# Kernel optimization log

Measured on AMD Instinct MI355X. Metric: run time of the kernel, lower is better.

Reference implementation:

```python
import jax, jax.numpy as jnp
import numpy as np

N_HEAD = 16

def _alibi_slopes(num_heads):
    # m_i = (256 ** (1/num_heads)) ** -(i+1)
    x = (2.0 ** 8) ** (1.0 / num_heads)
    return jnp.asarray([1.0 / x ** (i + 1) for i in range(num_heads)], dtype=jnp.float32)

def setup_inputs() -> dict:
    key = jax.random.key(0)
    k1, k2 = jax.random.split(key)
    B, S, D = 2, 2048, 1024
    x = jax.random.normal(k1, (B, S, D), dtype=jnp.float32)
    W_kqv = jax.random.normal(k2, (D, 3 * D), dtype=jnp.float32) * 0.02
    return {"x": x, "W_kqv": W_kqv}

def reference(x, W_kqv):
    B, S, D = x.shape
    H = N_HEAD
    hd = D // H
    scale = jnp.sqrt(jnp.asarray(D, dtype=x.dtype))  # NOTE: sqrt(n_embd), per source
    kqv = x @ W_kqv                                   # [B,S,3D]
    k, q, v = jnp.split(kqv, 3, axis=-1)              # chunk order: key, query, value
    q = q.reshape(B, S, H, hd).transpose(0, 2, 1, 3)  # [B,H,S,hd]
    k = k.reshape(B, S, H, hd).transpose(0, 2, 1, 3)
    v = v.reshape(B, S, H, hd).transpose(0, 2, 1, 3)
    # ALiBi bias: m[h] * (j - i)
    pos = jnp.arange(S)
    rel = (pos[None, :] - pos[:, None]).astype(x.dtype)      # [S,S]
    m = _alibi_slopes(H).astype(x.dtype)                     # [H]
    bias = m[:, None, None] * rel                            # [H,S,S]
    score = jnp.einsum('bhqd,bhkd->bhqk', q, k) / scale + bias[None]
    causal = pos[None, :] <= pos[:, None]                    # [S,S] lower-tri
    score = jnp.where(causal[None, None], score, -jnp.inf)
    attn = jax.nn.softmax(score, axis=-1)                    # [B,H,S,S]
    out = jnp.einsum('bhqk,bhkd->bhqd', attn, v)
    out = out.transpose(0, 2, 1, 3).reshape(B, S, D)
    return (out, attn)
```

## Files before the change

kernel.cpp:

```cpp
#include <hip/hip_runtime.h>
#include <hip/hip_bf16.h>

typedef __attribute__((ext_vector_type(8))) short short8;
typedef __attribute__((ext_vector_type(4))) float f32x4;

static __device__ __forceinline__ unsigned short f2bf(float f) {
    unsigned int x = __float_as_uint(f);
    x += 0x7fffu + ((x >> 16) & 1u);
    return (unsigned short)(x >> 16);
}

static __device__ __forceinline__ void gld_lds16(const unsigned short* g, unsigned short* l) {
    __builtin_amdgcn_global_load_lds((const __attribute__((address_space(1))) void*)g,
                                     (__attribute__((address_space(3))) void*)l, 16, 0, 0);
}

__global__ __launch_bounds__(256) void cvt_x_kernel(const float* __restrict__ in,
                                                    unsigned short* __restrict__ outb,
                                                    int n4) {
    int i = blockIdx.x * 256 + threadIdx.x;
    if (i < n4) {
        f32x4 v = *(const f32x4*)(in + (size_t)i * 4);
        ushort4 o;
        o.x = f2bf(v[0]); o.y = f2bf(v[1]); o.z = f2bf(v[2]); o.w = f2bf(v[3]);
        *(ushort4*)(outb + (size_t)i * 4) = o;
    }
}

__global__ __launch_bounds__(256) void cvt_wt_kernel(const float* __restrict__ W,
                                                     unsigned short* __restrict__ WT) {
    __shared__ float t[64][65];
    const int n0 = blockIdx.x * 64;
    const int k0 = blockIdx.y * 64;
    const int tid = threadIdx.x;
#pragma unroll
    for (int i = 0; i < 16; ++i) {
        int lin = tid + i * 256;
        int rr = lin >> 6, cc = lin & 63;
        t[rr][cc] = W[(size_t)(k0 + rr) * 3072 + n0 + cc];
    }
    __syncthreads();
#pragma unroll
    for (int i = 0; i < 16; ++i) {
        int lin = tid + i * 256;
        int nn = lin >> 6, kk = lin & 63;
        WT[(size_t)(n0 + nn) * 1024 + k0 + kk] = f2bf(t[kk][nn]);
    }
}

__global__ __launch_bounds__(256) void gemm_kqv_kernel(
    const unsigned short* __restrict__ A,
    const unsigned short* __restrict__ BT,
    unsigned short* __restrict__ qb,
    unsigned short* __restrict__ kb,
    unsigned short* __restrict__ vtb) {
    __shared__ __attribute__((aligned(16))) unsigned short smem[2 * 128 * 72];
    unsigned short (*As)[64] = (unsigned short(*)[64])smem;
    unsigned short (*Bs)[64] = (unsigned short(*)[64])(smem + 128 * 64);
    const int tid = threadIdx.x;
    const int w = tid >> 6, lane = tid & 63;
    const int quad = lane >> 4, cl = lane & 15;

    const int wg = (int)blockIdx.x + 24 * (int)blockIdx.y;
    const int wgs = (wg & 7) * 96 + (wg >> 3);
    const int m0 = (wgs / 24) * 128, n0 = (wgs % 24) * 128;
    const int wm = (w >> 1) * 64, wn = (w & 1) * 64;

    const int srow = lane >> 3;
    const int schk = (lane & 7) ^ srow;
    const unsigned short* Ap = A + (size_t)(m0 + w * 32 + srow) * 1024 + schk * 8;
    const unsigned short* Bp = BT + (size_t)(n0 + w * 32 + srow) * 1024 + schk * 8;

    f32x4 acc[4][4] = {};

    for (int kk = 0; kk < 1024; kk += 64) {
#pragma unroll
        for (int i = 0; i < 4; ++i) {
            gld_lds16(Ap + kk + (size_t)i * 8 * 1024, &As[w * 32 + i * 8][0]);
            gld_lds16(Bp + kk + (size_t)i * 8 * 1024, &Bs[w * 32 + i * 8][0]);
        }
        __syncthreads();
#pragma unroll
        for (int kc = 0; kc < 2; ++kc) {
            short8 af[4], bfr[4];
#pragma unroll
            for (int i = 0; i < 4; ++i) {
                const int col = ((kc * 4 + quad) ^ (cl & 7)) * 8;
                af[i] = *(const short8*)&As[wm + i * 16 + cl][col];
                bfr[i] = *(const short8*)&Bs[wn + i * 16 + cl][col];
            }
#pragma unroll
            for (int im = 0; im < 4; ++im)
#pragma unroll
                for (int in = 0; in < 4; ++in)
                    acc[im][in] = __builtin_amdgcn_mfma_f32_16x16x32_bf16(
                        af[im], bfr[in], acc[im][in], 0, 0, 0);
        }
        __syncthreads();
    }
    unsigned short (*Cs)[130] = (unsigned short(*)[130])smem;

    const int chunk = n0 >> 10;
    const int d0 = n0 & 1023;
    const int b = m0 >> 11;
    const int s_base = m0 & 2047;

    if (chunk == 2) {
#pragma unroll
        for (int im = 0; im < 4; ++im)
#pragma unroll
            for (int in = 0; in < 4; ++in)
#pragma unroll
                for (int rg = 0; rg < 4; ++rg)
                    Cs[wn + in * 16 + cl][wm + im * 16 + quad * 4 + rg] =
                        f2bf(acc[im][in][rg]);
        __syncthreads();
#pragma unroll
        for (int it = 0; it < 8; ++it) {
            int l = it * 2048 + tid * 8;
            int c = l >> 7;
            int r = l & 127;
            int d = d0 + c, hh = d >> 6, dd = d & 63;
            size_t dst = ((size_t)(b * 16 + hh) * 64 + dd) * 2048 + s_base + r;
            *(uint4*)(vtb + dst) = *(const uint4*)&Cs[c][r];
        }
    } else {
#pragma unroll
        for (int im = 0; im < 4; ++im)
#pragma unroll
            for (int in = 0; in < 4; ++in)
#pragma unroll
                for (int rg = 0; rg < 4; ++rg)
                    Cs[wm + im * 16 + quad * 4 + rg][wn + in * 16 + cl] =
                        f2bf(acc[im][in][rg]);
        __syncthreads();
        unsigned short* outp = (chunk == 0) ? kb : qb;
#pragma unroll
        for (int it = 0; it < 8; ++it) {
            int l = it * 2048 + tid * 8;
            int r = l >> 7;
            int c = l & 127;
            int d = d0 + c, hh = d >> 6, dd = d & 63;
            size_t dst = ((size_t)(b * 16 + hh) * 2048 + s_base + r) * 64 + dd;
            *(uint4*)(outp + dst) = *(const uint4*)&Cs[r][c];
        }
    }
}

__global__ __launch_bounds__(256, 4) void attn_kernel(
    const unsigned short* __restrict__ qb,
    const unsigned short* __restrict__ kb,
    const unsigned short* __restrict__ vtb,
    float* __restrict__ out_,
    float* __restrict__ attn) {
    const int h = blockIdx.y;
    const int b = blockIdx.z;
    const int bh = b * 16 + h;
    const int t64 = (23 * (int)blockIdx.x + 7 * bh) & 31;
    const int tid = threadIdx.x;
    const int w = tid >> 6;
    const int lane = tid & 63;
    const int quad = lane >> 4;
    const int cl = lane & 15;
    const int q0 = t64 * 64;
    const int row0 = q0 + w * 16;
    const int jtmax = t64;

    const unsigned short* Qh = qb + (size_t)bh * 2048 * 64;
    const unsigned short* Kh = kb + (size_t)bh * 2048 * 64;
    const unsigned short* Vh = vtb + (size_t)bh * 64 * 2048;
    float* attnh = attn + (size_t)bh * 2048 * 2048;

    __shared__ __attribute__((aligned(16))) unsigned short Kt[64][64];
    __shared__ __attribute__((aligned(16))) unsigned short Vt[64][64];
    __shared__ unsigned short Ps[4][16][72];

    const int srow = lane >> 3;
    const int schk = (lane & 7) ^ srow;

    short8 aq0 = *(const short8*)(Qh + (size_t)(row0 + cl) * 64 + quad * 8);
    short8 aq1 = *(const short8*)(Qh + (size_t)(row0 + cl) * 64 + 32 + quad * 8);

    const float mh = exp2f(-0.5f * (float)(h + 1));
    const float sc1 = 1.0f / 32.0f;

    float rsum[4] = {0.f, 0.f, 0.f, 0.f};
    for (int jt = 0; jt <= jtmax; ++jt) {
        const int j0 = jt * 64;
#pragma unroll
        for (int i = 0; i < 2; ++i)
            gld_lds16(Kh + (size_t)(j0 + w * 16 + i * 8 + srow) * 64 + schk * 8,
                      &Kt[w * 16 + i * 8][0]);
        __syncthreads();
#pragma unroll
        for (int nt = 0; nt < 4; ++nt) {
            const int r = nt * 16 + cl;
            short8 k0 = *(const short8*)&Kt[r][((quad) ^ (cl & 7)) * 8];
            short8 k1 = *(const short8*)&Kt[r][((quad + 4) ^ (cl & 7)) * 8];
            f32x4 s = {0.f, 0.f, 0.f, 0.f};
            s = __builtin_amdgcn_mfma_f32_16x16x32_bf16(aq0, k0, s, 0, 0, 0);
            s = __builtin_amdgcn_mfma_f32_16x16x32_bf16(aq1, k1, s, 0, 0, 0);
            const int jc = j0 + nt * 16 + cl;
#pragma unroll
            for (int rg = 0; rg < 4; ++rg) {
                int irow = row0 + quad * 4 + rg;
                if (jc <= irow)
                    rsum[rg] += __expf(s[rg] * sc1 + mh * (float)(jc - irow));
            }
        }
        __syncthreads();
    }
#pragma unroll
    for (int rg = 0; rg < 4; ++rg) {
        float v = rsum[rg];
        v += __shfl_xor(v, 1);
        v += __shfl_xor(v, 2);
        v += __shfl_xor(v, 4);
        v += __shfl_xor(v, 8);
        rsum[rg] = 1.0f / v;
    }

    f32x4 oacc[4] = {};
    for (int jt = 0; jt <= jtmax; ++jt) {
        const int j0 = jt * 64;
#pragma unroll
        for (int i = 0; i < 2; ++i) {
            gld_lds16(Kh + (size_t)(j0 + w * 16 + i * 8 + srow) * 64 + schk * 8,
                      &Kt[w * 16 + i * 8][0]);
            gld_lds16(Vh + (size_t)(w * 16 + i * 8 + srow) * 2048 + j0 + schk * 8,
                      &Vt[w * 16 + i * 8][0]);
        }
        __syncthreads();
        f32x4 sv[4];
#pragma unroll
        for (int nt = 0; nt < 4; ++nt) {
            const int r = nt * 16 + cl;
            short8 k0 = *(const short8*)&Kt[r][((quad) ^ (cl & 7)) * 8];
            short8 k1 = *(const short8*)&Kt[r][((quad + 4) ^ (cl & 7)) * 8];
            f32x4 s = {0.f, 0.f, 0.f, 0.f};
            s = __builtin_amdgcn_mfma_f32_16x16x32_bf16(aq0, k0, s, 0, 0, 0);
            sv[nt] = __builtin_amdgcn_mfma_f32_16x16x32_bf16(aq1, k1, s, 0, 0, 0);
        }
#pragma unroll
        for (int nt = 0; nt < 4; ++nt) {
            const int jc = j0 + nt * 16 + cl;
#pragma unroll
            for (int rg = 0; rg < 4; ++rg) {
                const int irow = row0 + quad * 4 + rg;
                float p = (jc <= irow)
                              ? __expf(sv[nt][rg] * sc1 + mh * (float)(jc - irow)) * rsum[rg]
                              : 0.f;
                Ps[w][quad * 4 + rg][nt * 16 + cl] = f2bf(p);
                __builtin_nontemporal_store(p, attnh + (size_t)irow * 2048 + jc);
            }
        }

        short8 pa0 = *(const short8*)&Ps[w][cl][quad * 8];
        short8 pa1 = *(const short8*)&Ps[w][cl][32 + quad * 8];

#pragma unroll
        for (int on = 0; on < 4; ++on) {
            const int r = on * 16 + cl;
            short8 v0 = *(const short8*)&Vt[r][((quad) ^ (cl & 7)) * 8];
            short8 v1 = *(const short8*)&Vt[r][((quad + 4) ^ (cl & 7)) * 8];
            oacc[on] = __builtin_amdgcn_mfma_f32_16x16x32_bf16(pa0, v0, oacc[on], 0, 0, 0);
            oacc[on] = __builtin_amdgcn_mfma_f32_16x16x32_bf16(pa1, v1, oacc[on], 0, 0, 0);
        }
        __syncthreads();
    }

#pragma unroll
    for (int on = 0; on < 4; ++on) {
#pragma unroll
        for (int rg = 0; rg < 4; ++rg) {
            int srow2 = row0 + quad * 4 + rg;
            __builtin_nontemporal_store(
                oacc[on][rg], out_ + ((size_t)b * 2048 + srow2) * 1024 + h * 64 + on * 16 + cl);
        }
    }

    const int jz = (jtmax + 1) * 64;
    if (jz < 2048) {
        f32x4 z = {0.f, 0.f, 0.f, 0.f};
        for (int rr = 0; rr < 16; ++rr) {
            float* dst = attnh + (size_t)(row0 + rr) * 2048;
            for (int c = jz + lane * 4; c < 2048; c += 256)
                __builtin_nontemporal_store(z, (f32x4*)(dst + c));
        }
    }
}

extern "C" void kernel_launch(void* const* d_in, const int* in_sizes, int n_in,
                              void* d_out, int out_size, void* d_ws, size_t ws_size,
                              hipStream_t stream) {
    const float* x = (const float*)d_in[0];
    const float* Wk = (const float*)d_in[1];
    float* out = (float*)d_out;
    float* attn = out + (size_t)2 * 2048 * 1024;

    unsigned short* xb = (unsigned short*)d_ws;
    unsigned short* wtb = xb + (size_t)4096 * 1024;
    unsigned short* qb = wtb + (size_t)3072 * 1024;
    unsigned short* kb = qb + (size_t)32 * 2048 * 64;
    unsigned short* vtb = kb + (size_t)32 * 2048 * 64;

    cvt_x_kernel<<<dim3(4096), dim3(256), 0, stream>>>(x, xb, 4096 * 1024 / 4);
    cvt_wt_kernel<<<dim3(48, 16), dim3(256), 0, stream>>>(Wk, wtb);
    gemm_kqv_kernel<<<dim3(24, 32), dim3(256), 0, stream>>>(xb, wtb, qb, kb, vtb);
    attn_kernel<<<dim3(32, 16, 2), dim3(256), 0, stream>>>(qb, kb, vtb, out, attn);
}
```

Measured before the change: 703.2 us.

## Double-buffer K/V tiles in LDS and XOR-swizzle the P staging buffer

```diff
diff --git a/kernel.cpp b/kernel.cpp
--- a/kernel.cpp
+++ b/kernel.cpp
@@ -171,13 +171,26 @@
     const unsigned short* Vh = vtb + (size_t)bh * 64 * 2048;
     float* attnh = attn + (size_t)bh * 2048 * 2048;
 
-    __shared__ __attribute__((aligned(16))) unsigned short Kt[64][64];
-    __shared__ __attribute__((aligned(16))) unsigned short Vt[64][64];
-    __shared__ unsigned short Ps[4][16][72];
+    __shared__ __attribute__((aligned(16))) unsigned short Kt[2][64][64];
+    __shared__ __attribute__((aligned(16))) unsigned short Vt[2][64][64];
+    __shared__ __attribute__((aligned(16))) unsigned short Ps[4][16][64];
 
     const int srow = lane >> 3;
     const int schk = (lane & 7) ^ srow;
 
+    auto stageK = [&](int jt, int buf) {
+#pragma unroll
+        for (int i = 0; i < 2; ++i)
+            gld_lds16(Kh + (size_t)(jt * 64 + w * 16 + i * 8 + srow) * 64 + schk * 8,
+                      &Kt[buf][w * 16 + i * 8][0]);
+    };
+    auto stageV = [&](int j0, int buf) {
+#pragma unroll
+        for (int i = 0; i < 2; ++i)
+            gld_lds16(Vh + (size_t)(w * 16 + i * 8 + srow) * 2048 + j0 + schk * 8,
+                      &Vt[buf][w * 16 + i * 8][0]);
+    };
+
     short8 aq0 = *(const short8*)(Qh + (size_t)(row0 + cl) * 64 + quad * 8);
     short8 aq1 = *(const short8*)(Qh + (size_t)(row0 + cl) * 64 + 32 + quad * 8);
 
@@ -185,30 +198,30 @@
     const float sc1 = 1.0f / 32.0f;
 
     float rsum[4] = {0.f, 0.f, 0.f, 0.f};
-    for (int jt = 0; jt <= jtmax; ++jt) {
-        const int j0 = jt * 64;
-#pragma unroll
-        for (int i = 0; i < 2; ++i)
-            gld_lds16(Kh + (size_t)(j0 + w * 16 + i * 8 + srow) * 64 + schk * 8,
-                      &Kt[w * 16 + i * 8][0]);
-        __syncthreads();
-#pragma unroll
-        for (int nt = 0; nt < 4; ++nt) {
-            const int r = nt * 16 + cl;
-            short8 k0 = *(const short8*)&Kt[r][((quad) ^ (cl & 7)) * 8];
-            short8 k1 = *(const short8*)&Kt[r][((quad + 4) ^ (cl & 7)) * 8];
-            f32x4 s = {0.f, 0.f, 0.f, 0.f};
-            s = __builtin_amdgcn_mfma_f32_16x16x32_bf16(aq0, k0, s, 0, 0, 0);
-            s = __builtin_amdgcn_mfma_f32_16x16x32_bf16(aq1, k1, s, 0, 0, 0);
-            const int jc = j0 + nt * 16 + cl;
-#pragma unroll
-            for (int rg = 0; rg < 4; ++rg) {
-                int irow = row0 + quad * 4 + rg;
-                if (jc <= irow)
-                    rsum[rg] += __expf(s[rg] * sc1 + mh * (float)(jc - irow));
-            }
-        }
-        __syncthreads();
+    stageK(0, 0);
+    {
+        int cur = 0;
+        for (int jt = 0; jt <= jtmax; ++jt, cur ^= 1) {
+            __syncthreads();
+            if (jt < jtmax) stageK(jt + 1, cur ^ 1);
+            const int j0 = jt * 64;
+#pragma unroll
+            for (int nt = 0; nt < 4; ++nt) {
+                const int r = nt * 16 + cl;
+                short8 k0 = *(const short8*)&Kt[cur][r][((quad) ^ (cl & 7)) * 8];
+                short8 k1 = *(const short8*)&Kt[cur][r][((quad + 4) ^ (cl & 7)) * 8];
+                f32x4 s = {0.f, 0.f, 0.f, 0.f};
+                s = __builtin_amdgcn_mfma_f32_16x16x32_bf16(aq0, k0, s, 0, 0, 0);
+                s = __builtin_amdgcn_mfma_f32_16x16x32_bf16(aq1, k1, s, 0, 0, 0);
+                const int jc = j0 + nt * 16 + cl;
+#pragma unroll
+                for (int rg = 0; rg < 4; ++rg) {
+                    int irow = row0 + quad * 4 + rg;
+                    if (jc <= irow)
+                        rsum[rg] += __expf(s[rg] * sc1 + mh * (float)(jc - irow));
+                }
+            }
+        }
     }
 #pragma unroll
     for (int rg = 0; rg < 4; ++rg) {
@@ -220,53 +233,57 @@
         rsum[rg] = 1.0f / v;
     }
 
+    __syncthreads();
     f32x4 oacc[4] = {};
-    for (int jt = 0; jt <= jtmax; ++jt) {
-        const int j0 = jt * 64;
-#pragma unroll
-        for (int i = 0; i < 2; ++i) {
-            gld_lds16(Kh + (size_t)(j0 + w * 16 + i * 8 + srow) * 64 + schk * 8,
-                      &Kt[w * 16 + i * 8][0]);
-            gld_lds16(Vh + (size_t)(w * 16 + i * 8 + srow) * 2048 + j0 + schk * 8,
-                      &Vt[w * 16 + i * 8][0]);
-        }
-        __syncthreads();
-        f32x4 sv[4];
-#pragma unroll
-        for (int nt = 0; nt < 4; ++nt) {
-            const int r = nt * 16 + cl;
-            short8 k0 = *(const short8*)&Kt[r][((quad) ^ (cl & 7)) * 8];
-            short8 k1 = *(const short8*)&Kt[r][((quad + 4) ^ (cl & 7)) * 8];
-            f32x4 s = {0.f, 0.f, 0.f, 0.f};
-            s = __builtin_amdgcn_mfma_f32_16x16x32_bf16(aq0, k0, s, 0, 0, 0);
-            sv[nt] = __builtin_amdgcn_mfma_f32_16x16x32_bf16(aq1, k1, s, 0, 0, 0);
-        }
-#pragma unroll
-        for (int nt = 0; nt < 4; ++nt) {
-            const int jc = j0 + nt * 16 + cl;
-#pragma unroll
-            for (int rg = 0; rg < 4; ++rg) {
-                const int irow = row0 + quad * 4 + rg;
-                float p = (jc <= irow)
-                              ? __expf(sv[nt][rg] * sc1 + mh * (float)(jc - irow)) * rsum[rg]
-                              : 0.f;
-                Ps[w][quad * 4 + rg][nt * 16 + cl] = f2bf(p);
-                __builtin_nontemporal_store(p, attnh + (size_t)irow * 2048 + jc);
-            }
-        }
-
-        short8 pa0 = *(const short8*)&Ps[w][cl][quad * 8];
-        short8 pa1 = *(const short8*)&Ps[w][cl][32 + quad * 8];
-
-#pragma unroll
-        for (int on = 0; on < 4; ++on) {
-            const int r = on * 16 + cl;
-            short8 v0 = *(const short8*)&Vt[r][((quad) ^ (cl & 7)) * 8];
-            short8 v1 = *(const short8*)&Vt[r][((quad + 4) ^ (cl & 7)) * 8];
-            oacc[on] = __builtin_amdgcn_mfma_f32_16x16x32_bf16(pa0, v0, oacc[on], 0, 0, 0);
-            oacc[on] = __builtin_amdgcn_mfma_f32_16x16x32_bf16(pa1, v1, oacc[on], 0, 0, 0);
-        }
-        __syncthreads();
+    stageK(0, 0);
+    stageV(0, 0);
+    {
+        int cur = 0;
+        for (int jt = 0; jt <= jtmax; ++jt, cur ^= 1) {
+            __syncthreads();
+            if (jt < jtmax) {
+                stageK(jt + 1, cur ^ 1);
+                stageV(jt * 64 + 64, cur ^ 1);
+            }
+            const int j0 = jt * 64;
+            f32x4 sv[4];
+#pragma unroll
+            for (int nt = 0; nt < 4; ++nt) {
+                const int r = nt * 16 + cl;
+                short8 k0 = *(const short8*)&Kt[cur][r][((quad) ^ (cl & 7)) * 8];
+                short8 k1 = *(const short8*)&Kt[cur][r][((quad + 4) ^ (cl & 7)) * 8];
+                f32x4 s = {0.f, 0.f, 0.f, 0.f};
+                s = __builtin_amdgcn_mfma_f32_16x16x32_bf16(aq0, k0, s, 0, 0, 0);
+                sv[nt] = __builtin_amdgcn_mfma_f32_16x16x32_bf16(aq1, k1, s, 0, 0, 0);
+            }
+#pragma unroll
+            for (int nt = 0; nt < 4; ++nt) {
+                const int jc = j0 + nt * 16 + cl;
+#pragma unroll
+                for (int rg = 0; rg < 4; ++rg) {
+                    const int irow = row0 + quad * 4 + rg;
+                    float p = (jc <= irow)
+                                  ? __expf(sv[nt][rg] * sc1 + mh * (float)(jc - irow)) * rsum[rg]
+                                  : 0.f;
+                    Ps[w][quad * 4 + rg]
+                      [(((nt * 2 + (cl >> 3)) ^ ((quad * 4 + rg) & 7)) << 3) | (cl & 7)] =
+                        f2bf(p);
+                    __builtin_nontemporal_store(p, attnh + (size_t)irow * 2048 + jc);
+                }
+            }
+
+            short8 pa0 = *(const short8*)&Ps[w][cl][((quad ^ (cl & 7)) << 3)];
+            short8 pa1 = *(const short8*)&Ps[w][cl][((((quad + 4)) ^ (cl & 7)) << 3)];
+
+#pragma unroll
+            for (int on = 0; on < 4; ++on) {
+                const int r = on * 16 + cl;
+                short8 v0 = *(const short8*)&Vt[cur][r][((quad) ^ (cl & 7)) * 8];
+                short8 v1 = *(const short8*)&Vt[cur][r][((quad + 4) ^ (cl & 7)) * 8];
+                oacc[on] = __builtin_amdgcn_mfma_f32_16x16x32_bf16(pa0, v0, oacc[on], 0, 0, 0);
+                oacc[on] = __builtin_amdgcn_mfma_f32_16x16x32_bf16(pa1, v1, oacc[on], 0, 0, 0);
+            }
+        }
     }
 
 #pragma unroll
```

Result: no change. 700.8 us (-0.3%).
